# Optimization experiments

Hardware: AMD Instinct MI355X
Metric: run time of the kernel (lower is better)

The kernel has to match this reference:

```python
import jax, jax.numpy as jnp
import numpy as np

B, S, D = 4, 4096, 2048
DC = D // 4       # complexity head hidden
DFF = 4 * D       # inner FFN hidden
MIN_CAP, MAX_CAP = 0.25, 1.0


def setup_inputs() -> dict:
    key = jax.random.key(0)
    ks = jax.random.split(key, 9)
    return {
        "hidden": jax.random.normal(ks[0], (B, S, D), jnp.float32),
        "router_weight": jax.random.normal(ks[1], (D,), jnp.float32) * 0.02,
        "router_bias": jnp.zeros((1,), jnp.float32),
        "comp_w1": jax.random.normal(ks[2], (D, DC), jnp.float32) * 0.02,
        "comp_b1": jnp.zeros((DC,), jnp.float32),
        "comp_w2": jax.random.normal(ks[3], (DC, 1), jnp.float32) * 0.02,
        "comp_b2": jnp.zeros((1,), jnp.float32),
        "ffn_w1": jax.random.normal(ks[4], (D, DFF), jnp.float32) * 0.02,
        "ffn_b1": jnp.zeros((DFF,), jnp.float32),
        "ffn_w2": jax.random.normal(ks[5], (DFF, D), jnp.float32) * 0.02,
        "ffn_b2": jnp.zeros((D,), jnp.float32),
    }


def reference(hidden, router_weight, router_bias, comp_w1, comp_b1, comp_w2,
              comp_b2, ffn_w1, ffn_b1, ffn_w2, ffn_b2):
    b, s, d = hidden.shape
    # complexity head on mean-pooled tokens -> scalar capacity (torch .item())
    pooled = hidden.mean(axis=1)                                   # [B, D]
    ch = jax.nn.gelu(pooled @ comp_w1 + comp_b1, approximate=False)
    complexity = jax.nn.sigmoid(ch @ comp_w2 + comp_b2)            # [B, 1]
    capacity = float(jnp.mean(MIN_CAP + complexity * (MAX_CAP - MIN_CAP)))
    k = int(capacity * s)
    if k == 0:
        return hidden
    # mod_top_k_routing: scalar router logits, per-sequence top-k tokens
    logits = jnp.einsum('bsd,d->bs', hidden, router_weight) + router_bias[0]
    top_logits, indices = jax.lax.top_k(logits, k)                 # [B, k]
    weights = jax.nn.sigmoid(top_logits)                           # [B, k]
    selected = jnp.take_along_axis(hidden, indices[:, :, None], axis=1)  # [B,k,D]
    # inner block: FFN d -> 4d -> d with GELU
    h = jax.nn.gelu(selected @ ffn_w1 + ffn_b1, approximate=False)
    processed = h @ ffn_w2 + ffn_b2                                # [B, k, D]
    # scatter_add weighted results back onto the residual stream
    weighted = processed * weights[:, :, None]
    b_idx = jnp.arange(b)[:, None]                                 # [B, 1]
    output = hidden.at[b_idx, indices].add(weighted)
    return output
```

## Files before the change

### kernel.cpp

```cpp
#include <hip/hip_runtime.h>
#include <hip/hip_bf16.h>
#include <math.h>

#define B_ 4
#define S_ 4096
#define D_ 2048
#define DC_ 512
#define DFF_ 8192

typedef __attribute__((ext_vector_type(8))) __bf16 bf16x8;
typedef __attribute__((ext_vector_type(4))) float f32x4;

__device__ __forceinline__ float gelu_exact(float x) {
    return 0.5f * x * (1.0f + erff(x * 0.70710678118654752f));
}

__device__ __forceinline__ unsigned short f2bf_bits(float f) {
    __hip_bfloat16 h = __float2bfloat16(f);
    return *reinterpret_cast<unsigned short*>(&h);
}

#define GLD16(gptr, lptr) \
    __builtin_amdgcn_global_load_lds( \
        (__attribute__((address_space(1))) void*)(gptr), \
        (__attribute__((address_space(3))) void*)(lptr), 16, 0, 0)

__global__ void pool_partial_k(const float* __restrict__ hidden, float* __restrict__ pp) {
    int d = blockIdx.x * 256 + threadIdx.x;
    int sc = blockIdx.y;
    int b = blockIdx.z;
    const float* base = hidden + ((size_t)b * S_ + (size_t)sc * 512) * D_ + d;
    float s = 0.f;
    #pragma unroll 4
    for (int i = 0; i < 512; ++i) s += base[(size_t)i * D_];
    pp[((size_t)sc * B_ + b) * D_ + d] = s;
}

__global__ void pool_reduce_k(const float* __restrict__ pp, float* __restrict__ pooled) {
    int tid = blockIdx.x * 256 + threadIdx.x;
    int b = tid >> 11;
    int d = tid & (D_ - 1);
    float s = 0.f;
    for (int sc = 0; sc < 8; ++sc) s += pp[((size_t)sc * B_ + b) * D_ + d];
    pooled[tid] = s * (1.0f / (float)S_);
}

__global__ __launch_bounds__(256) void logits_k(const float* __restrict__ hidden,
                                                const float* __restrict__ rw,
                                                const float* __restrict__ rb,
                                                float* __restrict__ logits) {
    int tok = blockIdx.x * 4 + (threadIdx.x >> 6);
    int lane = threadIdx.x & 63;
    const float4* row = (const float4*)(hidden + (size_t)tok * D_);
    const float4* w4 = (const float4*)rw;
    float s = 0.f;
    #pragma unroll
    for (int i = 0; i < 8; ++i) {
        float4 v = row[i * 64 + lane];
        float4 w = w4[i * 64 + lane];
        s += (v.x * w.x + v.y * w.y) + (v.z * w.z + v.w * w.w);
    }
    #pragma unroll
    for (int off = 32; off > 0; off >>= 1) s += __shfl_down(s, off, 64);
    if (lane == 0) logits[tok] = s + rb[0];
}

__global__ void head1_k(const float* __restrict__ pooled, const float* __restrict__ w1,
                        const float* __restrict__ b1, float* __restrict__ ch) {
    int j = blockIdx.x * 256 + threadIdx.x;
    int b = j >> 9, c = j & (DC_ - 1);
    float acc = 0.f;
    for (int i = 0; i < D_; ++i) acc += pooled[b * D_ + i] * w1[(size_t)i * DC_ + c];
    ch[j] = gelu_exact(acc + b1[c]);
}

__global__ void head2_k(const float* __restrict__ ch, const float* __restrict__ w2,
                        const float* __restrict__ b2, int* __restrict__ kbuf) {
    __shared__ float red[4];
    int t = threadIdx.x;
    int b = t >> 6, lane = t & 63;
    float acc = 0.f;
    #pragma unroll
    for (int i = 0; i < 8; ++i) acc += ch[b * DC_ + i * 64 + lane] * w2[i * 64 + lane];
    #pragma unroll
    for (int off = 32; off > 0; off >>= 1) acc += __shfl_down(acc, off, 64);
    if (lane == 0) {
        float z = acc + b2[0];
        float cx = 1.f / (1.f + expf(-z));
        red[b] = 0.25f + cx * 0.75f;
    }
    __syncthreads();
    if (t == 0) {
        float cap = ((red[0] + red[1]) + (red[2] + red[3])) * 0.25f;
        int kk = (int)((double)cap * (double)S_);
        if (kk < 0) kk = 0;
        if (kk > S_) kk = S_;
        kbuf[0] = kk;
    }
}

__global__ __launch_bounds__(256) void select_k(const float* __restrict__ logits,
                                                const int* __restrict__ kbuf,
                                                int* __restrict__ gidx,
                                                float* __restrict__ gwt) {
    int b = blockIdx.x;
    int t = threadIdx.x;
    int k = kbuf[0];
    __shared__ float slog[S_];
    __shared__ unsigned su[S_];
    __shared__ int hist[256];
    __shared__ unsigned sprefix;
    __shared__ int srem;
    __shared__ int sg[256], se[256];

    for (int i = t; i < S_; i += 256) {
        float f = logits[b * S_ + i];
        slog[i] = f;
        unsigned ub = __float_as_uint(f);
        su[i] = (ub & 0x80000000u) ? ~ub : (ub | 0x80000000u);
    }
    if (t == 0) { sprefix = 0u; srem = k; }
    __syncthreads();

    for (int round = 0; round < 4; ++round) {
        int shift = 24 - round * 8;
        hist[t] = 0;
        __syncthreads();
        unsigned pref = sprefix;
        unsigned pmask = (round == 0) ? 0u : ~((1u << (shift + 8)) - 1u);
        for (int i = t; i < S_; i += 256) {
            unsigned u = su[i];
            if ((u & pmask) == (pref & pmask))
                atomicAdd(&hist[(u >> shift) & 255], 1);
        }
        __syncthreads();
        if (t == 0) {
            int rem = srem, run = 0;
            for (int v = 255; v >= 0; --v) {
                int h = hist[v];
                if (run + h >= rem) {
                    srem = rem - run;
                    sprefix = pref | ((unsigned)v << shift);
                    break;
                }
                run += h;
            }
        }
        __syncthreads();
    }
    unsigned T = sprefix;
    int need_eq = srem;

    int base = t * 16;
    int local_gt = 0, local_eq = 0;
    #pragma unroll
    for (int i = 0; i < 16; ++i) {
        unsigned u = su[base + i];
        local_gt += (u > T);
        local_eq += (u == T);
    }
    sg[t] = local_gt; se[t] = local_eq;
    __syncthreads();
    for (int o = 1; o < 256; o <<= 1) {
        int vg = (t >= o) ? sg[t - o] : 0;
        int ve = (t >= o) ? se[t - o] : 0;
        __syncthreads();
        sg[t] += vg; se[t] += ve;
        __syncthreads();
    }
    int gt_excl = sg[t] - local_gt;
    int eq_excl = se[t] - local_eq;
    int total_gt = sg[255];

    int gpos = gt_excl, epos = eq_excl;
    for (int i = 0; i < 16; ++i) {
        int s = base + i;
        unsigned u = su[s];
        int pos = -1;
        if (u > T) pos = gpos++;
        else if (u == T) { if (epos < need_eq) pos = total_gt + epos; epos++; }
        if (pos >= 0) {
            gidx[b * k + pos] = b * S_ + s;
            gwt[b * k + pos] = 1.f / (1.f + expf(-slog[s]));
        }
    }
}

__global__ void gather_k(const float* __restrict__ hidden, const int* __restrict__ gidx,
                         const int* __restrict__ kbuf, __hip_bfloat16* __restrict__ Ag) {
    int tid = blockIdx.x * 256 + threadIdx.x;
    int m = tid >> 9, c4 = tid & 511;
    int M = B_ * kbuf[0];
    if (m >= M) return;
    int row = gidx[m];
    float4 v = ((const float4*)(hidden + (size_t)row * D_))[c4];
    ushort4 o;
    o.x = f2bf_bits(v.x); o.y = f2bf_bits(v.y); o.z = f2bf_bits(v.z); o.w = f2bf_bits(v.w);
    ((ushort4*)Ag)[tid] = o;
}

__global__ void transpose_cvt_k(const float* __restrict__ in, __hip_bfloat16* __restrict__ out,
                                int R, int C) {
    __shared__ float tile[32][33];
    int r0 = blockIdx.y * 32, c0 = blockIdx.x * 32;
    int tx = threadIdx.x, ty = threadIdx.y;
    #pragma unroll
    for (int i = 0; i < 32; i += 8)
        tile[ty + i][tx] = in[(size_t)(r0 + ty + i) * C + (c0 + tx)];
    __syncthreads();
    #pragma unroll
    for (int i = 0; i < 32; i += 8)
        out[(size_t)(c0 + ty + i) * R + (r0 + tx)] = __float2bfloat16(tile[tx][ty + i]);
}


#define FENCE_() asm volatile("" ::: "memory")
#define BARR_()  do { FENCE_(); __builtin_amdgcn_s_barrier(); FENCE_(); } while (0)
#define VMW_()   do { if constexpr (BN == 256) asm volatile("s_waitcnt vmcnt(6)" ::: "memory"); \
                      else                     asm volatile("s_waitcnt vmcnt(5)" ::: "memory"); \
                      __builtin_amdgcn_sched_barrier(0); } while (0)

template <int BN, int EPI>
__global__ __launch_bounds__(512, 2) void gemm8p(
    const __hip_bfloat16* __restrict__ A, int lda,
    const __hip_bfloat16* __restrict__ BT, int ldb,
    const float* __restrict__ bias,
    __hip_bfloat16* __restrict__ Hout, int ldh,
    float* __restrict__ out,
    const int* __restrict__ gidx, const float* __restrict__ gwt,
    const int* __restrict__ kbuf, int K, int first)
{
    constexpr int NQ = BN / 128;
    constexpr int NF = 2 * NQ;
    constexpr int BUFB = BN * 128;
    extern __shared__ char lds[];

    const int M = B_ * kbuf[0];
    const int m0 = blockIdx.y * 256;
    if (m0 >= M) return;
    const int n0 = blockIdx.x * BN;

    const int t = threadIdx.x;
    const int lane = t & 63;
    const int wave = t >> 6;
    const int wr = wave >> 2, wc = wave & 3;

    const int rl = t >> 3;
    const int cbs = ((t & 7) << 4) ^ ((rl & 7) << 4);
    const int wchunk = (t >> 6) << 10;

    bf16x8 aR[4][2], bR[NQ][2];
    f32x4 acc[8][NF] = {};

    auto STG = [&](const __hip_bfloat16* src, int row0, int rowMax, int kcol,
                   int ld, int ldsoff) {
        int gr = row0 + rl;
        if (gr > rowMax) gr = rowMax;
        GLD16(src + (size_t)gr * ld + (kcol + (cbs >> 1)), lds + ldsoff + wchunk);
    };
    auto SA = [&](int buf, int h, int kt) {
        int bo = buf * 32768 + h * 16384;
        STG(A, m0 + h * 128,      M - 1, kt * 64, lda, bo);
        STG(A, m0 + h * 128 + 64, M - 1, kt * 64, lda, bo + 8192);
    };
    auto SB = [&](int buf, int v, int kt) {
        int bo = 65536 + buf * BUFB + v * (BUFB / 2);
        if constexpr (BN == 256) {
            STG(BT, n0 + v * 128,      0x7fffffff, kt * 64, ldb, bo);
            STG(BT, n0 + v * 128 + 64, 0x7fffffff, kt * 64, ldb, bo + 8192);
        } else {
            STG(BT, n0 + v * 64, 0x7fffffff, kt * 64, ldb, bo);
        }
    };
    auto RA = [&](int buf, int h) {
        int bo = buf * 32768;
        #pragma unroll
        for (int q = 0; q < 4; ++q) {
            int row = h * 128 + wr * 64 + q * 16 + (lane & 15);
            int ro = bo + row * 128;
            int sw = (row & 7) << 4;
            #pragma unroll
            for (int ks = 0; ks < 2; ++ks)
                aR[q][ks] = *(const bf16x8*)(lds + ro + ((ks * 64 + ((lane >> 4) << 4)) ^ sw));
        }
    };
    auto RB = [&](int buf, int v) {
        int bo = 65536 + buf * BUFB;
        #pragma unroll
        for (int q = 0; q < NQ; ++q) {
            int row = v * (BN / 2) + wc * (BN / 8) + q * 16 + (lane & 15);
            int ro = bo + row * 128;
            int sw = (row & 7) << 4;
            #pragma unroll
            for (int ks = 0; ks < 2; ++ks)
                bR[q][ks] = *(const bf16x8*)(lds + ro + ((ks * 64 + ((lane >> 4) << 4)) ^ sw));
        }
    };
    auto MM = [&](int h, int v) {
        __builtin_amdgcn_s_setprio(1);
        #pragma unroll
        for (int mi = 0; mi < 4; ++mi)
            #pragma unroll
            for (int nj = 0; nj < NQ; ++nj)
                #pragma unroll
                for (int ks = 0; ks < 2; ++ks)
                    acc[h * 4 + mi][v * NQ + nj] = __builtin_amdgcn_mfma_f32_16x16x32_bf16(
                        aR[mi][ks], bR[nj][ks], acc[h * 4 + mi][v * NQ + nj], 0, 0, 0);
        __builtin_amdgcn_s_setprio(0);
    };

    const int nkt = K >> 6;
    const int nit = K >> 7;

    SA(0, 0, 0); SA(0, 1, 0); SB(0, 0, 0); SB(0, 1, 0);
    SA(1, 0, 1); SB(1, 1, 1); SA(1, 1, 1);
    VMW_(); BARR_();

    for (int it = 0; it < nit; ++it) {
        int k1 = 2 * it + 1;
        int k2 = 2 * it + 2; if (k2 > nkt - 1) k2 = nkt - 1;
        int k3 = 2 * it + 3; if (k3 > nkt - 1) k3 = nkt - 1;
        RA(0, 0); RB(0, 0); SB(1, 0, k1); BARR_(); MM(0, 0); BARR_();
        RB(0, 1);           SA(0, 0, k2); BARR_(); MM(0, 1); BARR_();
        RA(0, 1);           SB(0, 1, k2); BARR_(); MM(1, 1); BARR_();
        RB(0, 0);           SA(0, 1, k2); BARR_(); MM(1, 0); VMW_(); BARR_();
        RA(1, 0); RB(1, 0); SB(0, 0, k2); BARR_(); MM(0, 0); BARR_();
        RB(1, 1);           SA(1, 0, k3); BARR_(); MM(0, 1); BARR_();
        RA(1, 1);           SB(1, 1, k3); BARR_(); MM(1, 1); BARR_();
        RB(1, 0);           SA(1, 1, k3); BARR_(); MM(1, 0); VMW_(); BARR_();
    }
    asm volatile("s_waitcnt vmcnt(0)" ::: "memory");

    const int qrow = (lane >> 4) << 2, qcol = lane & 15;
    #pragma unroll
    for (int f = 0; f < 8; ++f) {
        const int h = f >> 2, mi = f & 3;
        const int mbase = m0 + h * 128 + wr * 64 + mi * 16 + qrow;
        if constexpr (EPI == 0) {
            #pragma unroll
            for (int g = 0; g < NF; ++g) {
                const int v = g / NQ, nj = g % NQ;
                const int col = n0 + v * (BN / 2) + wc * (BN / 8) + nj * 16 + qcol;
                const float bv = bias[col];
                #pragma unroll
                for (int r = 0; r < 4; ++r) {
                    int m = mbase + r;
                    if (m < M)
                        Hout[(size_t)m * ldh + col] =
                            __float2bfloat16(gelu_exact(acc[f][g][r] + bv));
                }
            }
        } else {
            #pragma unroll
            for (int r = 0; r < 4; ++r) {
                int m = mbase + r;
                if (m < M) {
                    int grow = gidx[m];
                    float wgt = gwt[m];
                    float* orow = out + (size_t)grow * D_;
                    #pragma unroll
                    for (int g = 0; g < NF; ++g) {
                        const int v = g / NQ, nj = g % NQ;
                        const int col = n0 + v * (BN / 2) + wc * (BN / 8) + nj * 16 + qcol;
                        float vv = acc[f][g][r];
                        if (first) vv += bias[col];
                        orow[col] += wgt * vv;
                    }
                }
            }
        }
    }
}

extern "C" void kernel_launch(void* const* d_in, const int* in_sizes, int n_in,
                              void* d_out, int out_size, void* d_ws, size_t ws_size,
                              hipStream_t stream) {
    (void)in_sizes; (void)n_in;
    const float* hidden = (const float*)d_in[0];
    const float* rw  = (const float*)d_in[1];
    const float* rb  = (const float*)d_in[2];
    const float* cw1 = (const float*)d_in[3];
    const float* cb1 = (const float*)d_in[4];
    const float* cw2 = (const float*)d_in[5];
    const float* cb2 = (const float*)d_in[6];
    const float* fw1 = (const float*)d_in[7];
    const float* fb1 = (const float*)d_in[8];
    const float* fw2 = (const float*)d_in[9];
    const float* fb2 = (const float*)d_in[10];

    char* ws = (char*)d_ws;
    size_t off = 0;
    auto alloc = [&](size_t bytes) {
        size_t r = (off + 255) & ~(size_t)255;
        off = r + bytes;
        return r;
    };
    size_t o_logits = alloc((size_t)B_ * S_ * 4);
    size_t o_pp     = alloc((size_t)8 * B_ * D_ * 4);
    size_t o_pooled = alloc((size_t)B_ * D_ * 4);
    size_t o_ch     = alloc((size_t)B_ * DC_ * 4);
    size_t o_k      = alloc(256);
    size_t o_gidx   = alloc((size_t)B_ * S_ * 4);
    size_t o_gwt    = alloc((size_t)B_ * S_ * 4);
    size_t o_w1T    = alloc((size_t)D_ * DFF_ * 2);
    size_t o_w2T    = alloc((size_t)D_ * DFF_ * 2);
    size_t o_Ag     = alloc((size_t)B_ * S_ * D_ * 2);
    size_t base     = (off + 255) & ~(size_t)255;
    int CH = DFF_;
    while (CH > 256 && base + (size_t)B_ * S_ * CH * 2 > ws_size) CH >>= 1;
    size_t o_H = alloc((size_t)B_ * S_ * CH * 2);

    float* logits = (float*)(ws + o_logits);
    float* pp     = (float*)(ws + o_pp);
    float* pooled = (float*)(ws + o_pooled);
    float* ch     = (float*)(ws + o_ch);
    int*   kbuf   = (int*)(ws + o_k);
    int*   gidx   = (int*)(ws + o_gidx);
    float* gwt    = (float*)(ws + o_gwt);
    __hip_bfloat16* w1T = (__hip_bfloat16*)(ws + o_w1T);
    __hip_bfloat16* w2T = (__hip_bfloat16*)(ws + o_w2T);
    __hip_bfloat16* Ag  = (__hip_bfloat16*)(ws + o_Ag);
    __hip_bfloat16* H   = (__hip_bfloat16*)(ws + o_H);
    float* out = (float*)d_out;

    hipError_t e;
    e = hipFuncSetAttribute((const void*)gemm8p<256, 0>,
                            hipFuncAttributeMaxDynamicSharedMemorySize, 131072);
    e = hipFuncSetAttribute((const void*)gemm8p<128, 1>,
                            hipFuncAttributeMaxDynamicSharedMemorySize, 131072);
    (void)e;

    pool_partial_k<<<dim3(D_ / 256, 8, B_), 256, 0, stream>>>(hidden, pp);
    pool_reduce_k<<<dim3(B_ * D_ / 256), 256, 0, stream>>>(pp, pooled);
    logits_k<<<dim3(B_ * S_ / 4), 256, 0, stream>>>(hidden, rw, rb, logits);
    head1_k<<<dim3(B_ * DC_ / 256), 256, 0, stream>>>(pooled, cw1, cb1, ch);
    head2_k<<<dim3(1), 256, 0, stream>>>(ch, cw2, cb2, kbuf);
    select_k<<<dim3(B_), 256, 0, stream>>>(logits, kbuf, gidx, gwt);
    gather_k<<<dim3(B_ * S_ * (D_ / 4) / 256), 256, 0, stream>>>(hidden, gidx, kbuf, Ag);
    transpose_cvt_k<<<dim3(DFF_ / 32, D_ / 32), dim3(32, 8), 0, stream>>>(fw1, w1T, D_, DFF_);
    transpose_cvt_k<<<dim3(D_ / 32, DFF_ / 32), dim3(32, 8), 0, stream>>>(fw2, w2T, DFF_, D_);
    hipMemcpyAsync(d_out, (const void*)hidden, (size_t)out_size * 4,
                   hipMemcpyDeviceToDevice, stream);

    int nch = DFF_ / CH;
    for (int c = 0; c < nch; ++c) {
        gemm8p<256, 0><<<dim3(CH / 256, B_ * S_ / 256), 512, 131072, stream>>>(
            Ag, D_, w1T + (size_t)c * CH * D_, D_, fb1 + c * CH,
            H, CH, nullptr, nullptr, nullptr, kbuf, D_, 0);
        gemm8p<128, 1><<<dim3(D_ / 128, B_ * S_ / 256), 512, 98304, stream>>>(
            H, CH, w2T + (size_t)c * CH, DFF_, fb2,
            nullptr, 0, out, gidx, gwt, kbuf, CH, c == 0);
    }
}
```

Baseline: 1.576 ms.

## Replace direct global-to-LDS loads with register-staged loads and LDS writes in GEMM

After: 1.737 ms. +10.2%, slower.

```diff
diff --git a/kernel.cpp b/kernel.cpp
--- a/kernel.cpp
+++ b/kernel.cpp
@@ -19,11 +19,6 @@
     __hip_bfloat16 h = __float2bfloat16(f);
     return *reinterpret_cast<unsigned short*>(&h);
 }
-
-#define GLD16(gptr, lptr) \
-    __builtin_amdgcn_global_load_lds( \
-        (__attribute__((address_space(1))) void*)(gptr), \
-        (__attribute__((address_space(3))) void*)(lptr), 16, 0, 0)
 
 __global__ void pool_partial_k(const float* __restrict__ hidden, float* __restrict__ pp) {
     int d = blockIdx.x * 256 + threadIdx.x;
@@ -216,8 +211,7 @@
 
 #define FENCE_() asm volatile("" ::: "memory")
 #define BARR_()  do { FENCE_(); __builtin_amdgcn_s_barrier(); FENCE_(); } while (0)
-#define VMW_()   do { if constexpr (BN == 256) asm volatile("s_waitcnt vmcnt(6)" ::: "memory"); \
-                      else                     asm volatile("s_waitcnt vmcnt(5)" ::: "memory"); \
+#define LKW_()   do { asm volatile("s_waitcnt lgkmcnt(0)" ::: "memory"); \
                       __builtin_amdgcn_sched_barrier(0); } while (0)
 
 template <int BN, int EPI>
@@ -245,32 +239,42 @@
     const int wave = t >> 6;
     const int wr = wave >> 2, wc = wave & 3;
 
-    const int rl = t >> 3;
-    const int cbs = ((t & 7) << 4) ^ ((rl & 7) << 4);
-    const int wchunk = (t >> 6) << 10;
+    const int rl  = t >> 3;
+    const int cb  = (t & 7) << 4;
+    const int wsw = cb ^ ((rl & 7) << 4);
+    const int ce  = cb >> 1;
 
     bf16x8 aR[4][2], bR[NQ][2];
     f32x4 acc[8][NF] = {};
-
-    auto STG = [&](const __hip_bfloat16* src, int row0, int rowMax, int kcol,
-                   int ld, int ldsoff) {
-        int gr = row0 + rl;
-        if (gr > rowMax) gr = rowMax;
-        GLD16(src + (size_t)gr * ld + (kcol + (cbs >> 1)), lds + ldsoff + wchunk);
-    };
-    auto SA = [&](int buf, int h, int kt) {
-        int bo = buf * 32768 + h * 16384;
-        STG(A, m0 + h * 128,      M - 1, kt * 64, lda, bo);
-        STG(A, m0 + h * 128 + 64, M - 1, kt * 64, lda, bo + 8192);
-    };
-    auto SB = [&](int buf, int v, int kt) {
-        int bo = 65536 + buf * BUFB + v * (BUFB / 2);
+    bf16x8 S0a, S0b, S1a, S1b, S2a, S2b, S3a, S3b;
+
+    auto LA = [&](bf16x8& ra, bf16x8& rb, int h, int kt) {
+        int r0 = m0 + h * 128 + rl;      if (r0 >= M) r0 = M - 1;
+        int r1 = m0 + h * 128 + 64 + rl; if (r1 >= M) r1 = M - 1;
+        const __hip_bfloat16* p = A + (size_t)kt * 64 + ce;
+        ra = *(const bf16x8*)(p + (size_t)r0 * lda);
+        rb = *(const bf16x8*)(p + (size_t)r1 * lda);
+    };
+    auto LB = [&](bf16x8& ra, bf16x8& rb, int v, int kt) {
+        const __hip_bfloat16* p = BT + (size_t)kt * 64 + ce;
         if constexpr (BN == 256) {
-            STG(BT, n0 + v * 128,      0x7fffffff, kt * 64, ldb, bo);
-            STG(BT, n0 + v * 128 + 64, 0x7fffffff, kt * 64, ldb, bo + 8192);
+            ra = *(const bf16x8*)(p + (size_t)(n0 + v * 128 + rl) * ldb);
+            rb = *(const bf16x8*)(p + (size_t)(n0 + v * 128 + 64 + rl) * ldb);
         } else {
-            STG(BT, n0 + v * 64, 0x7fffffff, kt * 64, ldb, bo);
-        }
+            ra = *(const bf16x8*)(p + (size_t)(n0 + v * 64 + rl) * ldb);
+            (void)rb;
+        }
+    };
+    auto WA = [&](const bf16x8& ra, const bf16x8& rb, int buf, int h) {
+        char* base = lds + buf * 32768 + h * 16384;
+        *(bf16x8*)(base + rl * 128 + wsw) = ra;
+        *(bf16x8*)(base + 8192 + rl * 128 + wsw) = rb;
+    };
+    auto WB = [&](const bf16x8& ra, const bf16x8& rb, int buf, int v) {
+        char* base = lds + 65536 + buf * BUFB + v * (BUFB / 2);
+        *(bf16x8*)(base + rl * 128 + wsw) = ra;
+        if constexpr (BN == 256)
+            *(bf16x8*)(base + 8192 + rl * 128 + wsw) = rb;
     };
     auto RA = [&](int buf, int h) {
         int bo = buf * 32768;
@@ -311,25 +315,41 @@
 
     const int nkt = K >> 6;
     const int nit = K >> 7;
-
-    SA(0, 0, 0); SA(0, 1, 0); SB(0, 0, 0); SB(0, 1, 0);
-    SA(1, 0, 1); SB(1, 1, 1); SA(1, 1, 1);
-    VMW_(); BARR_();
+    const int kl = nkt - 1;
+
+    {
+        int kp1 = (1 <= kl) ? 1 : kl;
+        int kp2 = (2 <= kl) ? 2 : kl;
+        LA(S0a, S0b, 0, 0); LA(S1a, S1b, 1, 0); LB(S2a, S2b, 0, 0); LB(S3a, S3b, 1, 0);
+        WA(S0a, S0b, 0, 0); WA(S1a, S1b, 0, 1); WB(S2a, S2b, 0, 0); WB(S3a, S3b, 0, 1);
+        LA(S0a, S0b, 0, kp1); LB(S1a, S1b, 1, kp1); LA(S2a, S2b, 1, kp1);
+        WA(S0a, S0b, 1, 0); WB(S1a, S1b, 1, 1); WA(S2a, S2b, 1, 1);
+        LB(S2a, S2b, 0, kp1);
+        LA(S3a, S3b, 0, kp2);
+    }
+    LKW_(); BARR_();
 
     for (int it = 0; it < nit; ++it) {
-        int k1 = 2 * it + 1;
-        int k2 = 2 * it + 2; if (k2 > nkt - 1) k2 = nkt - 1;
-        int k3 = 2 * it + 3; if (k3 > nkt - 1) k3 = nkt - 1;
-        RA(0, 0); RB(0, 0); SB(1, 0, k1); BARR_(); MM(0, 0); BARR_();
-        RB(0, 1);           SA(0, 0, k2); BARR_(); MM(0, 1); BARR_();
-        RA(0, 1);           SB(0, 1, k2); BARR_(); MM(1, 1); BARR_();
-        RB(0, 0);           SA(0, 1, k2); BARR_(); MM(1, 0); VMW_(); BARR_();
-        RA(1, 0); RB(1, 0); SB(0, 0, k2); BARR_(); MM(0, 0); BARR_();
-        RB(1, 1);           SA(1, 0, k3); BARR_(); MM(0, 1); BARR_();
-        RA(1, 1);           SB(1, 1, k3); BARR_(); MM(1, 1); BARR_();
-        RB(1, 0);           SA(1, 1, k3); BARR_(); MM(1, 0); VMW_(); BARR_();
-    }
-    asm volatile("s_waitcnt vmcnt(0)" ::: "memory");
+        int k2 = 2 * it + 2; if (k2 > kl) k2 = kl;
+        int k3 = 2 * it + 3; if (k3 > kl) k3 = kl;
+        int k4 = 2 * it + 4; if (k4 > kl) k4 = kl;
+        RA(0, 0); RB(0, 0); WB(S2a, S2b, 1, 0); LB(S0a, S0b, 1, k2);
+        LKW_(); BARR_(); MM(0, 0); BARR_();
+        RB(0, 1);           WA(S3a, S3b, 0, 0); LA(S1a, S1b, 1, k2);
+        LKW_(); BARR_(); MM(0, 1); BARR_();
+        RA(0, 1);           WB(S0a, S0b, 0, 1); LB(S2a, S2b, 0, k2);
+        LKW_(); BARR_(); MM(1, 1); BARR_();
+        RB(0, 0);           WA(S1a, S1b, 0, 1); LA(S3a, S3b, 0, k3);
+        LKW_(); BARR_(); MM(1, 0); BARR_();
+        RA(1, 0); RB(1, 0); WB(S2a, S2b, 0, 0); LB(S0a, S0b, 1, k3);
+        LKW_(); BARR_(); MM(0, 0); BARR_();
+        RB(1, 1);           WA(S3a, S3b, 1, 0); LA(S1a, S1b, 1, k3);
+        LKW_(); BARR_(); MM(0, 1); BARR_();
+        RA(1, 1);           WB(S0a, S0b, 1, 1); LB(S2a, S2b, 0, k3);
+        LKW_(); BARR_(); MM(1, 1); BARR_();
+        RB(1, 0);           WA(S1a, S1b, 1, 1); LA(S3a, S3b, 0, k4);
+        LKW_(); BARR_(); MM(1, 0); BARR_();
+    }
 
     const int qrow = (lane >> 4) << 2, qcol = lane & 15;
     #pragma unroll
```

## Widen down-proj GEMM tile, add XCD block swizzle, split-K complexity head

Applied to the files above, without the earlier changes.

Result: no change. 1.547 ms (-1.9%).

```diff
diff --git a/kernel.cpp b/kernel.cpp
--- a/kernel.cpp
+++ b/kernel.cpp
@@ -65,13 +65,26 @@
     if (lane == 0) logits[tok] = s + rb[0];
 }
 
-__global__ void head1_k(const float* __restrict__ pooled, const float* __restrict__ w1,
-                        const float* __restrict__ b1, float* __restrict__ ch) {
-    int j = blockIdx.x * 256 + threadIdx.x;
-    int b = j >> 9, c = j & (DC_ - 1);
+__global__ __launch_bounds__(256) void head1_k(const float* __restrict__ pooled,
+                                               const float* __restrict__ w1,
+                                               const float* __restrict__ b1,
+                                               float* __restrict__ ch) {
+    __shared__ float red[256];
+    int b = blockIdx.y;
+    int cl = threadIdx.x & 63;
+    int c = blockIdx.x * 64 + cl;
+    int ks = threadIdx.x >> 6;
+    const float* pr = pooled + b * D_ + ks * 512;
+    const float* wp = w1 + (size_t)(ks * 512) * DC_ + c;
     float acc = 0.f;
-    for (int i = 0; i < D_; ++i) acc += pooled[b * D_ + i] * w1[(size_t)i * DC_ + c];
-    ch[j] = gelu_exact(acc + b1[c]);
+    #pragma unroll 8
+    for (int i = 0; i < 512; ++i) acc += pr[i] * wp[(size_t)i * DC_];
+    red[threadIdx.x] = acc;
+    __syncthreads();
+    if (ks == 0) {
+        float s = ((red[cl] + red[cl + 64]) + (red[cl + 128] + red[cl + 192]));
+        ch[b * DC_ + c] = gelu_exact(s + b1[c]);
+    }
 }
 
 __global__ void head2_k(const float* __restrict__ ch, const float* __restrict__ w2,
@@ -216,11 +229,10 @@
 
 #define FENCE_() asm volatile("" ::: "memory")
 #define BARR_()  do { FENCE_(); __builtin_amdgcn_s_barrier(); FENCE_(); } while (0)
-#define VMW_()   do { if constexpr (BN == 256) asm volatile("s_waitcnt vmcnt(6)" ::: "memory"); \
-                      else                     asm volatile("s_waitcnt vmcnt(5)" ::: "memory"); \
+#define VMW_()   do { asm volatile("s_waitcnt vmcnt(6)" ::: "memory"); \
                       __builtin_amdgcn_sched_barrier(0); } while (0)
 
-template <int BN, int EPI>
+template <int BN, int EPI, int SWZ>
 __global__ __launch_bounds__(512, 2) void gemm8p(
     const __hip_bfloat16* __restrict__ A, int lda,
     const __hip_bfloat16* __restrict__ BT, int ldb,
@@ -236,9 +248,17 @@
     extern __shared__ char lds[];
 
     const int M = B_ * kbuf[0];
-    const int m0 = blockIdx.y * 256;
+    int bx = blockIdx.x, by = blockIdx.y;
+    if constexpr (SWZ) {
+        const int nwg = gridDim.x * gridDim.y;
+        int flat = by * gridDim.x + bx;
+        flat = (flat & 7) * (nwg >> 3) + (flat >> 3);
+        bx = flat % gridDim.x;
+        by = flat / gridDim.x;
+    }
+    const int m0 = by * 256;
     if (m0 >= M) return;
-    const int n0 = blockIdx.x * BN;
+    const int n0 = bx * BN;
 
     const int t = threadIdx.x;
     const int lane = t & 63;
@@ -424,16 +444,16 @@
     float* out = (float*)d_out;
 
     hipError_t e;
-    e = hipFuncSetAttribute((const void*)gemm8p<256, 0>,
+    e = hipFuncSetAttribute((const void*)gemm8p<256, 0, 0>,
                             hipFuncAttributeMaxDynamicSharedMemorySize, 131072);
-    e = hipFuncSetAttribute((const void*)gemm8p<128, 1>,
+    e = hipFuncSetAttribute((const void*)gemm8p<256, 1, 1>,
                             hipFuncAttributeMaxDynamicSharedMemorySize, 131072);
     (void)e;
 
     pool_partial_k<<<dim3(D_ / 256, 8, B_), 256, 0, stream>>>(hidden, pp);
     pool_reduce_k<<<dim3(B_ * D_ / 256), 256, 0, stream>>>(pp, pooled);
     logits_k<<<dim3(B_ * S_ / 4), 256, 0, stream>>>(hidden, rw, rb, logits);
-    head1_k<<<dim3(B_ * DC_ / 256), 256, 0, stream>>>(pooled, cw1, cb1, ch);
+    head1_k<<<dim3(DC_ / 64, B_), 256, 0, stream>>>(pooled, cw1, cb1, ch);
     head2_k<<<dim3(1), 256, 0, stream>>>(ch, cw2, cb2, kbuf);
     select_k<<<dim3(B_), 256, 0, stream>>>(logits, kbuf, gidx, gwt);
     gather_k<<<dim3(B_ * S_ * (D_ / 4) / 256), 256, 0, stream>>>(hidden, gidx, kbuf, Ag);
@@ -444,10 +464,10 @@
 
     int nch = DFF_ / CH;
     for (int c = 0; c < nch; ++c) {
-        gemm8p<256, 0><<<dim3(CH / 256, B_ * S_ / 256), 512, 131072, stream>>>(
+        gemm8p<256, 0, 0><<<dim3(CH / 256, B_ * S_ / 256), 512, 131072, stream>>>(
             Ag, D_, w1T + (size_t)c * CH * D_, D_, fb1 + c * CH,
             H, CH, nullptr, nullptr, nullptr, kbuf, D_, 0);
-        gemm8p<128, 1><<<dim3(D_ / 128, B_ * S_ / 256), 512, 98304, stream>>>(
+        gemm8p<256, 1, 1><<<dim3(D_ / 256, B_ * S_ / 256), 512, 131072, stream>>>(
             H, CH, w2T + (size_t)c * CH, DFF_, fb2,
             nullptr, 0, out, gidx, gwt, kbuf, CH, c == 0);
     }
```
